# Kernel tuning notes

Measured on AMD Instinct MI355X. Metric: run time of the kernel, lower is better.

The kernel has to match this reference:

```python
import jax, jax.numpy as jnp
import numpy as np

B, L, I, O = 32, 512, 1024, 1024
TMIN, TMAX = -8.0, -2.0


def setup_inputs() -> dict:
    key = jax.random.key(0)
    k1, k2, k3, k4, k5 = jax.random.split(key, 5)
    x = jax.random.normal(k1, (B, L, I), dtype=jnp.float32)
    weight_mean = jax.random.normal(k2, (O, I), dtype=jnp.float32) * 0.02
    # matches torch init: -rand * (tmax - tmin) + tmin
    weight_logvar = -jax.random.uniform(k3, (O, I), dtype=jnp.float32) * (TMAX - TMIN) + TMIN
    bias = jax.random.normal(k4, (O,), dtype=jnp.float32) * 0.02
    # standard-normal reparameterization noise (the torch module's randn)
    noise = jax.random.normal(k5, (B, O, I), dtype=jnp.float32)
    return {"x": x, "weight_mean": weight_mean, "weight_logvar": weight_logvar,
            "bias": bias, "noise": noise}


def reference(x, weight_mean, weight_logvar, bias, noise):
    # per-sample sampled weights: W_b = mean + eps_b * sqrt(exp(logvar))
    w = weight_mean + noise * jnp.exp(0.5 * weight_logvar)  # (B, O, I)
    # bmm(x, W^T) + bias  ->  (B, L, O)
    return jnp.einsum('bli,boi->blo', x, w) + bias
```

## Files before the change

### kernel.cpp

```cpp
#include <hip/hip_runtime.h>
#include <hip/hip_bf16.h>
#include <stdint.h>

#define B_ 32
#define L_ 512
#define I_ 1024
#define O_ 1024
#define NSTEP (I_ / 32)

typedef float  f32x4  __attribute__((ext_vector_type(4)));
typedef __bf16 bf16x4 __attribute__((ext_vector_type(4)));
typedef __bf16 bf16x8 __attribute__((ext_vector_type(8)));

__device__ __forceinline__ void gload_lds16(const void* g, void* l) {
    __builtin_amdgcn_global_load_lds(
        (const __attribute__((address_space(1))) uint32_t*)(uintptr_t)g,
        (__attribute__((address_space(3))) uint32_t*)(uint32_t)(uintptr_t)l,
        16, 0, 0);
}

__global__ void gen_w_kernel(const float* __restrict__ wmean,
                             const float* __restrict__ wlv,
                             const float* __restrict__ noise,
                             __bf16* __restrict__ W)
{
    const int n4 = B_ * O_ * I_ / 4;
    const int stride = gridDim.x * blockDim.x;
    for (int i = blockIdx.x * blockDim.x + threadIdx.x; i < n4; i += stride) {
        const int mi = i & (O_ * I_ / 4 - 1);
        const f32x4 m4 = *(const f32x4*)(wmean + (size_t)mi * 4);
        const f32x4 l4 = *(const f32x4*)(wlv   + (size_t)mi * 4);
        const f32x4 e4 = *(const f32x4*)(noise + (size_t)i  * 4);
        bf16x4 w;
        w[0] = (__bf16)(m4[0] + e4[0] * __expf(0.5f * l4[0]));
        w[1] = (__bf16)(m4[1] + e4[1] * __expf(0.5f * l4[1]));
        w[2] = (__bf16)(m4[2] + e4[2] * __expf(0.5f * l4[2]));
        w[3] = (__bf16)(m4[3] + e4[3] * __expf(0.5f * l4[3]));
        *(bf16x4*)(W + (size_t)i * 4) = w;
    }
}

__global__ void cvt_x_kernel(const float* __restrict__ x, __bf16* __restrict__ xb)
{
    const int n4 = B_ * L_ * I_ / 4;
    const int stride = gridDim.x * blockDim.x;
    for (int i = blockIdx.x * blockDim.x + threadIdx.x; i < n4; i += stride) {
        const f32x4 v = *(const f32x4*)(x + (size_t)i * 4);
        bf16x4 w;
        w[0] = (__bf16)v[0]; w[1] = (__bf16)v[1];
        w[2] = (__bf16)v[2]; w[3] = (__bf16)v[3];
        *(bf16x4*)(xb + (size_t)i * 4) = w;
    }
}

__global__ __launch_bounds__(256) void gemm_2ph(const __bf16* __restrict__ xb,
                                                const __bf16* __restrict__ W,
                                                const float* __restrict__ bias,
                                                float* __restrict__ out)
{
    __shared__ __bf16 As[2][128 * 32];
    __shared__ __bf16 Bs[2][128 * 32];

    const int bid = ((int)blockIdx.x & 7) * 128 + ((int)blockIdx.x >> 3);
    const int b   = bid >> 5;
    const int mt  = (bid >> 3) & 3;
    const int nt  = bid & 7;

    const int t    = threadIdx.x;
    const int wave = t >> 6, lane = t & 63;
    const int wr   = wave >> 1, wc = wave & 1;
    const int hr   = lane & 15, kq = lane >> 4;

    const __bf16* xrow = xb + (size_t)b * L_ * I_ + (size_t)(mt * 128) * I_;
    const __bf16* wrow = W  + (size_t)b * O_ * I_ + (size_t)(nt * 128) * I_;

    const int r1 = t >> 2, q1 = t & 3;
    const size_t goff1 = (size_t)r1 * I_ + q1 * 8;
    const size_t goff2 = (size_t)(r1 + 64) * I_ + q1 * 8;

    f32x4 acc[4][4];
    #pragma unroll
    for (int m = 0; m < 4; ++m)
        #pragma unroll
        for (int n = 0; n < 4; ++n)
            acc[m][n] = (f32x4)(0.0f);

    gload_lds16(xrow + goff1, &As[0][t * 8]);
    gload_lds16(wrow + goff1, &Bs[0][t * 8]);
    gload_lds16(xrow + goff2, &As[0][t * 8 + 2048]);
    gload_lds16(wrow + goff2, &Bs[0][t * 8 + 2048]);
    __syncthreads();

    int cur = 0;
    for (int it = 0; it < NSTEP; ++it) {
        if (it + 1 < NSTEP) {
            const int k0n = (it + 1) * 32;
            const int nxt = cur ^ 1;
            gload_lds16(xrow + goff1 + k0n, &As[nxt][t * 8]);
            gload_lds16(wrow + goff1 + k0n, &Bs[nxt][t * 8]);
            gload_lds16(xrow + goff2 + k0n, &As[nxt][t * 8 + 2048]);
            gload_lds16(wrow + goff2 + k0n, &Bs[nxt][t * 8 + 2048]);
        }

        bf16x8 af[4], bfr[4];
        #pragma unroll
        for (int m = 0; m < 4; ++m)
            af[m] = *(const bf16x8*)&As[cur][(wr * 64 + m * 16 + hr) * 32 + kq * 8];
        #pragma unroll
        for (int n = 0; n < 4; ++n)
            bfr[n] = *(const bf16x8*)&Bs[cur][(wc * 64 + n * 16 + hr) * 32 + kq * 8];
        #pragma unroll
        for (int m = 0; m < 4; ++m)
            #pragma unroll
            for (int n = 0; n < 4; ++n)
                acc[m][n] = __builtin_amdgcn_mfma_f32_16x16x32_bf16(af[m], bfr[n], acc[m][n], 0, 0, 0);

        __syncthreads();
        cur ^= 1;
    }

    float* ob = out + (size_t)b * L_ * O_;
    #pragma unroll
    for (int n = 0; n < 4; ++n) {
        const int col = nt * 128 + wc * 64 + n * 16 + hr;
        const float bv = bias[col];
        #pragma unroll
        for (int m = 0; m < 4; ++m) {
            const int row0 = mt * 128 + wr * 64 + m * 16 + kq * 4;
            #pragma unroll
            for (int j = 0; j < 4; ++j)
                ob[(size_t)(row0 + j) * O_ + col] = acc[m][n][j] + bv;
        }
    }
}

#define LDSPAD 40
__global__ void bayes_gemm_fused(const float* __restrict__ x,
                                 const float* __restrict__ wmean,
                                 const float* __restrict__ wlogvar,
                                 const float* __restrict__ bias,
                                 const float* __restrict__ noise,
                                 float* __restrict__ out)
{
    __shared__ __bf16 As[128 * LDSPAD];
    __shared__ __bf16 Bs[128 * LDSPAD];
    const int bid  = blockIdx.x;
    const int b    = bid >> 5;
    const int mt   = (bid >> 3) & 3;
    const int nt   = bid & 7;
    const int t    = threadIdx.x;
    const int wave = t >> 6, lane = t & 63;
    const int wr   = wave >> 1, wc = wave & 1;
    const int hr   = lane & 15, kq = lane >> 4;
    const float* xb = x     + (size_t)b * L_ * I_;
    const float* nb = noise + (size_t)b * O_ * I_;
    f32x4 acc[4][4];
    #pragma unroll
    for (int m = 0; m < 4; ++m)
        #pragma unroll
        for (int n = 0; n < 4; ++n) acc[m][n] = (f32x4)(0.0f);
    for (int k0 = 0; k0 < I_; k0 += 32) {
        #pragma unroll
        for (int j = 0; j < 4; ++j) {
            const int s = t + j * 256, row = s >> 3, q = s & 7;
            const float4 v = *(const float4*)(xb + (size_t)(mt * 128 + row) * I_ + k0 + q * 4);
            __bf16* dst = &As[row * LDSPAD + q * 4];
            dst[0] = (__bf16)v.x; dst[1] = (__bf16)v.y; dst[2] = (__bf16)v.z; dst[3] = (__bf16)v.w;
        }
        #pragma unroll
        for (int j = 0; j < 4; ++j) {
            const int s = t + j * 256, row = s >> 3, q = s & 7;
            const size_t off = (size_t)(nt * 128 + row) * I_ + k0 + q * 4;
            const float4 m4 = *(const float4*)(wmean + off);
            const float4 l4 = *(const float4*)(wlogvar + off);
            const float4 n4 = *(const float4*)(nb + off);
            __bf16* dst = &Bs[row * LDSPAD + q * 4];
            dst[0] = (__bf16)(m4.x + n4.x * __expf(0.5f * l4.x));
            dst[1] = (__bf16)(m4.y + n4.y * __expf(0.5f * l4.y));
            dst[2] = (__bf16)(m4.z + n4.z * __expf(0.5f * l4.z));
            dst[3] = (__bf16)(m4.w + n4.w * __expf(0.5f * l4.w));
        }
        __syncthreads();
        bf16x8 af[4], bfr[4];
        #pragma unroll
        for (int m = 0; m < 4; ++m)
            af[m] = *(const bf16x8*)&As[(wr * 64 + m * 16 + hr) * LDSPAD + kq * 8];
        #pragma unroll
        for (int n = 0; n < 4; ++n)
            bfr[n] = *(const bf16x8*)&Bs[(wc * 64 + n * 16 + hr) * LDSPAD + kq * 8];
        #pragma unroll
        for (int m = 0; m < 4; ++m)
            #pragma unroll
            for (int n = 0; n < 4; ++n)
                acc[m][n] = __builtin_amdgcn_mfma_f32_16x16x32_bf16(af[m], bfr[n], acc[m][n], 0, 0, 0);
        __syncthreads();
    }
    float* ob = out + (size_t)b * L_ * O_;
    #pragma unroll
    for (int n = 0; n < 4; ++n) {
        const int col = nt * 128 + wc * 64 + n * 16 + hr;
        const float bv = bias[col];
        #pragma unroll
        for (int m = 0; m < 4; ++m) {
            const int row0 = mt * 128 + wr * 64 + m * 16 + kq * 4;
            #pragma unroll
            for (int j = 0; j < 4; ++j)
                ob[(size_t)(row0 + j) * O_ + col] = acc[m][n][j] + bv;
        }
    }
}

extern "C" void kernel_launch(void* const* d_in, const int* in_sizes, int n_in,
                              void* d_out, int out_size, void* d_ws, size_t ws_size,
                              hipStream_t stream) {
    const float* x       = (const float*)d_in[0];
    const float* wmean   = (const float*)d_in[1];
    const float* wlogvar = (const float*)d_in[2];
    const float* bias    = (const float*)d_in[3];
    const float* noise   = (const float*)d_in[4];
    float* out           = (float*)d_out;

    const size_t w_bytes  = (size_t)B_ * O_ * I_ * 2;
    const size_t xb_bytes = (size_t)B_ * L_ * I_ * 2;

    if (ws_size >= w_bytes + xb_bytes) {
        __bf16* W  = (__bf16*)d_ws;
        __bf16* xb = (__bf16*)((char*)d_ws + w_bytes);
        gen_w_kernel<<<dim3(2048), dim3(256), 0, stream>>>(wmean, wlogvar, noise, W);
        cvt_x_kernel<<<dim3(1024), dim3(256), 0, stream>>>(x, xb);
        gemm_2ph<<<dim3(1024), dim3(256), 0, stream>>>(xb, W, bias, out);
    } else {
        bayes_gemm_fused<<<dim3(1024), dim3(256), 0, stream>>>(
            x, wmean, wlogvar, bias, noise, out);
    }
}
```

Measured before the change: 124.6 us.

## Rewrite bf16 GEMM with 256x256 tiles, 4-stage LDS ring and swizzle

Replaces the double-buffered 128x128 GEMM with a 256x256 tile kernel of 512 threads. It uses a four-deep LDS ring fed by async global-to-LDS loads, explicit vmcnt waits and a single barrier per k-step. The LDS layout is XOR-swizzled to avoid bank conflicts, and s_setprio is raised around the MFMA block. The aim is higher data reuse per tile and better overlap of loads with matrix math. In exchange it uses more LDS and registers and launches only 256 blocks, which may leave some compute units underused.

Result: faster. 113.8 us (-8.7%).

```diff
diff --git a/kernel.cpp b/kernel.cpp
--- a/kernel.cpp
+++ b/kernel.cpp
@@ -6,7 +6,8 @@
 #define L_ 512
 #define I_ 1024
 #define O_ 1024
-#define NSTEP (I_ / 32)
+#define BK 32
+#define NT (I_ / BK)
 
 typedef float  f32x4  __attribute__((ext_vector_type(4)));
 typedef __bf16 bf16x4 __attribute__((ext_vector_type(4)));
@@ -53,80 +54,94 @@
     }
 }
 
-__global__ __launch_bounds__(256) void gemm_2ph(const __bf16* __restrict__ xb,
-                                                const __bf16* __restrict__ W,
-                                                const float* __restrict__ bias,
-                                                float* __restrict__ out)
-{
-    __shared__ __bf16 As[2][128 * 32];
-    __shared__ __bf16 Bs[2][128 * 32];
-
-    const int bid = ((int)blockIdx.x & 7) * 128 + ((int)blockIdx.x >> 3);
-    const int b   = bid >> 5;
-    const int mt  = (bid >> 3) & 3;
-    const int nt  = bid & 7;
-
-    const int t    = threadIdx.x;
-    const int wave = t >> 6, lane = t & 63;
-    const int wr   = wave >> 1, wc = wave & 1;
-    const int hr   = lane & 15, kq = lane >> 4;
-
-    const __bf16* xrow = xb + (size_t)b * L_ * I_ + (size_t)(mt * 128) * I_;
-    const __bf16* wrow = W  + (size_t)b * O_ * I_ + (size_t)(nt * 128) * I_;
-
-    const int r1 = t >> 2, q1 = t & 3;
-    const size_t goff1 = (size_t)r1 * I_ + q1 * 8;
-    const size_t goff2 = (size_t)(r1 + 64) * I_ + q1 * 8;
-
-    f32x4 acc[4][4];
-    #pragma unroll
-    for (int m = 0; m < 4; ++m)
+__global__ __launch_bounds__(512, 2) void gemm_ring(const __bf16* __restrict__ xb,
+                                                    const __bf16* __restrict__ W,
+                                                    const float* __restrict__ bias,
+                                                    float* __restrict__ out)
+{
+    __shared__ __bf16 Abuf[4][256 * BK];
+    __shared__ __bf16 Bbuf[4][256 * BK];
+
+    const int bid = ((int)blockIdx.x & 7) * 32 + ((int)blockIdx.x >> 3);
+    const int b   = bid >> 3;
+    const int mt  = (bid >> 2) & 1;
+    const int nt  = bid & 3;
+
+    const int tid  = threadIdx.x;
+    const int wid  = tid >> 6, lane = tid & 63;
+    const int wr   = wid >> 2;
+    const int wc   = wid & 3;
+    const int hr   = lane & 15;
+    const int kq   = lane >> 4;
+
+    const int rowS = tid >> 2;
+    const int pcS  = tid & 3;
+    const int cS   = pcS ^ ((rowS >> 1) & 3);
+    const __bf16* ga = xb + (size_t)b * L_ * I_ + (size_t)(mt * 256 + rowS) * I_ + cS * 8;
+    const __bf16* gb = W  + (size_t)b * O_ * I_ + (size_t)(nt * 256 + rowS) * I_ + cS * 8;
+    const size_t ghalf = (size_t)128 * I_;
+
+#define STAGE(kt_) {                                                        \
+        const int bsel_ = (kt_) & 3;                                        \
+        const int ko_   = (kt_) * BK;                                       \
+        gload_lds16(ga + ko_,         &Abuf[bsel_][tid * 8]);               \
+        gload_lds16(ga + ko_ + ghalf, &Abuf[bsel_][tid * 8 + 4096]);        \
+        gload_lds16(gb + ko_,         &Bbuf[bsel_][tid * 8]);               \
+        gload_lds16(gb + ko_ + ghalf, &Bbuf[bsel_][tid * 8 + 4096]);        \
+    }
+
+    const int xorv = (hr >> 1) & 3;
+    const int pch  = kq ^ xorv;
+    const int aoff = (wr * 128 + hr) * 64 + pch * 16;
+    const int boff = (wc * 64  + hr) * 64 + pch * 16;
+
+    f32x4 acc[8][4];
+    #pragma unroll
+    for (int m = 0; m < 8; ++m)
         #pragma unroll
         for (int n = 0; n < 4; ++n)
             acc[m][n] = (f32x4)(0.0f);
 
-    gload_lds16(xrow + goff1, &As[0][t * 8]);
-    gload_lds16(wrow + goff1, &Bs[0][t * 8]);
-    gload_lds16(xrow + goff2, &As[0][t * 8 + 2048]);
-    gload_lds16(wrow + goff2, &Bs[0][t * 8 + 2048]);
-    __syncthreads();
-
-    int cur = 0;
-    for (int it = 0; it < NSTEP; ++it) {
-        if (it + 1 < NSTEP) {
-            const int k0n = (it + 1) * 32;
-            const int nxt = cur ^ 1;
-            gload_lds16(xrow + goff1 + k0n, &As[nxt][t * 8]);
-            gload_lds16(wrow + goff1 + k0n, &Bs[nxt][t * 8]);
-            gload_lds16(xrow + goff2 + k0n, &As[nxt][t * 8 + 2048]);
-            gload_lds16(wrow + goff2 + k0n, &Bs[nxt][t * 8 + 2048]);
-        }
-
-        bf16x8 af[4], bfr[4];
-        #pragma unroll
-        for (int m = 0; m < 4; ++m)
-            af[m] = *(const bf16x8*)&As[cur][(wr * 64 + m * 16 + hr) * 32 + kq * 8];
+    STAGE(0); STAGE(1); STAGE(2);
+
+    for (int kt = 0; kt < NT; ++kt) {
+        if (kt <= NT - 3)      asm volatile("s_waitcnt vmcnt(8)" ::: "memory");
+        else if (kt == NT - 2) asm volatile("s_waitcnt vmcnt(4)" ::: "memory");
+        else                   asm volatile("s_waitcnt vmcnt(0)" ::: "memory");
+        __builtin_amdgcn_s_barrier();
+        asm volatile("" ::: "memory");
+
+        if (kt + 3 < NT) STAGE(kt + 3);
+
+        const char* As = (const char*)&Abuf[kt & 3][0];
+        const char* Bs = (const char*)&Bbuf[kt & 3][0];
+
+        bf16x8 af[8], bfr[4];
+        #pragma unroll
+        for (int m = 0; m < 8; ++m)
+            af[m] = *(const bf16x8*)(As + aoff + m * 1024);
         #pragma unroll
         for (int n = 0; n < 4; ++n)
-            bfr[n] = *(const bf16x8*)&Bs[cur][(wc * 64 + n * 16 + hr) * 32 + kq * 8];
-        #pragma unroll
-        for (int m = 0; m < 4; ++m)
+            bfr[n] = *(const bf16x8*)(Bs + boff + n * 1024);
+
+        __builtin_amdgcn_s_setprio(1);
+        #pragma unroll
+        for (int m = 0; m < 8; ++m)
             #pragma unroll
             for (int n = 0; n < 4; ++n)
                 acc[m][n] = __builtin_amdgcn_mfma_f32_16x16x32_bf16(af[m], bfr[n], acc[m][n], 0, 0, 0);
-
-        __syncthreads();
-        cur ^= 1;
-    }
+        __builtin_amdgcn_s_setprio(0);
+    }
+#undef STAGE
 
     float* ob = out + (size_t)b * L_ * O_;
     #pragma unroll
     for (int n = 0; n < 4; ++n) {
-        const int col = nt * 128 + wc * 64 + n * 16 + hr;
+        const int col = nt * 256 + wc * 64 + n * 16 + hr;
         const float bv = bias[col];
         #pragma unroll
-        for (int m = 0; m < 4; ++m) {
-            const int row0 = mt * 128 + wr * 64 + m * 16 + kq * 4;
+        for (int m = 0; m < 8; ++m) {
+            const int row0 = mt * 256 + wr * 128 + m * 16 + kq * 4;
             #pragma unroll
             for (int j = 0; j < 4; ++j)
                 ob[(size_t)(row0 + j) * O_ + col] = acc[m][n][j] + bv;
@@ -225,10 +240,10 @@
 
     if (ws_size >= w_bytes + xb_bytes) {
         __bf16* W  = (__bf16*)d_ws;
-        __bf16* xb = (__bf16*)((char*)d_ws + w_bytes);
+        __bf16* xbuf = (__bf16*)((char*)d_ws + w_bytes);
         gen_w_kernel<<<dim3(2048), dim3(256), 0, stream>>>(wmean, wlogvar, noise, W);
-        cvt_x_kernel<<<dim3(1024), dim3(256), 0, stream>>>(x, xb);
-        gemm_2ph<<<dim3(1024), dim3(256), 0, stream>>>(xb, W, bias, out);
+        cvt_x_kernel<<<dim3(1024), dim3(256), 0, stream>>>(x, xbuf);
+        gemm_ring<<<dim3(256), dim3(512), 0, stream>>>(xbuf, W, bias, out);
     } else {
         bayes_gemm_fused<<<dim3(1024), dim3(256), 0, stream>>>(
             x, wmean, wlogvar, bias, noise, out);
```

## Fuse weight sampling and x conversion into GEMM with precomputed bf16 mean/sigma

Applied to the files above, without the earlier changes.

Replaces the three-kernel pipeline (materialize sampled bf16 W for all batches, convert x to bf16, then GEMM) with a small kernel that precomputes bf16 mean and sigma once, plus a fused GEMM. The fused GEMM reads fp32 x and noise directly, forms the sampled weights in registers, and writes bf16 tiles to double-buffered padded LDS. It uses 512-thread blocks, an LDS-staged coalesced epilogue, and raised wave priority around the MFMAs. This removes the large intermediate W and xb writes and re-reads. The cost is extra per-tile conversion work inside the GEMM and register-staged loads in place of direct global-to-LDS loads. Rounding mean and sigma to bf16 before combining them also slightly changes precision.

Result: slower. 136.4 us (+9.5%).

```diff
diff --git a/kernel.cpp b/kernel.cpp
--- a/kernel.cpp
+++ b/kernel.cpp
@@ -6,130 +6,158 @@
 #define L_ 512
 #define I_ 1024
 #define O_ 1024
-#define NSTEP (I_ / 32)
-
-typedef float  f32x4  __attribute__((ext_vector_type(4)));
+#define NST 32
+
+typedef float  f32x4 __attribute__((ext_vector_type(4)));
+typedef float  f32x2 __attribute__((ext_vector_type(2)));
 typedef __bf16 bf16x4 __attribute__((ext_vector_type(4)));
 typedef __bf16 bf16x8 __attribute__((ext_vector_type(8)));
 
-__device__ __forceinline__ void gload_lds16(const void* g, void* l) {
-    __builtin_amdgcn_global_load_lds(
-        (const __attribute__((address_space(1))) uint32_t*)(uintptr_t)g,
-        (__attribute__((address_space(3))) uint32_t*)(uint32_t)(uintptr_t)l,
-        16, 0, 0);
-}
-
-__global__ void gen_w_kernel(const float* __restrict__ wmean,
-                             const float* __restrict__ wlv,
-                             const float* __restrict__ noise,
-                             __bf16* __restrict__ W)
+#define CFENCE() asm volatile("" ::: "memory")
+#define BARRIER() do { CFENCE(); __builtin_amdgcn_s_barrier(); CFENCE(); } while (0)
+#define LGKM0()  asm volatile("s_waitcnt lgkmcnt(0)" ::: "memory")
+
+__global__ void gen_ms_kernel(const float* __restrict__ wmean, const float* __restrict__ wlv,
+                              __bf16* __restrict__ mz, __bf16* __restrict__ sgm)
 {
-    const int n4 = B_ * O_ * I_ / 4;
-    const int stride = gridDim.x * blockDim.x;
-    for (int i = blockIdx.x * blockDim.x + threadIdx.x; i < n4; i += stride) {
-        const int mi = i & (O_ * I_ / 4 - 1);
-        const f32x4 m4 = *(const f32x4*)(wmean + (size_t)mi * 4);
-        const f32x4 l4 = *(const f32x4*)(wlv   + (size_t)mi * 4);
-        const f32x4 e4 = *(const f32x4*)(noise + (size_t)i  * 4);
-        bf16x4 w;
-        w[0] = (__bf16)(m4[0] + e4[0] * __expf(0.5f * l4[0]));
-        w[1] = (__bf16)(m4[1] + e4[1] * __expf(0.5f * l4[1]));
-        w[2] = (__bf16)(m4[2] + e4[2] * __expf(0.5f * l4[2]));
-        w[3] = (__bf16)(m4[3] + e4[3] * __expf(0.5f * l4[3]));
-        *(bf16x4*)(W + (size_t)i * 4) = w;
-    }
-}
-
-__global__ void cvt_x_kernel(const float* __restrict__ x, __bf16* __restrict__ xb)
+    const int i = blockIdx.x * blockDim.x + threadIdx.x;
+    const f32x4 m = *(const f32x4*)(wmean + (size_t)i * 4);
+    const f32x4 l = *(const f32x4*)(wlv   + (size_t)i * 4);
+    bf16x4 mb, sb;
+    #pragma unroll
+    for (int e = 0; e < 4; ++e) {
+        mb[e] = (__bf16)m[e];
+        sb[e] = (__bf16)__expf(0.5f * l[e]);
+    }
+    *(bf16x4*)(mz  + (size_t)i * 4) = mb;
+    *(bf16x4*)(sgm + (size_t)i * 4) = sb;
+}
+
+__global__ __launch_bounds__(512, 4) void fused_gemm(const float* __restrict__ x,
+                                                     const float* __restrict__ noise,
+                                                     const __bf16* __restrict__ mz,
+                                                     const __bf16* __restrict__ sgm,
+                                                     const float* __restrict__ bias,
+                                                     float* __restrict__ out)
 {
-    const int n4 = B_ * L_ * I_ / 4;
-    const int stride = gridDim.x * blockDim.x;
-    for (int i = blockIdx.x * blockDim.x + threadIdx.x; i < n4; i += stride) {
-        const f32x4 v = *(const f32x4*)(x + (size_t)i * 4);
-        bf16x4 w;
-        w[0] = (__bf16)v[0]; w[1] = (__bf16)v[1];
-        w[2] = (__bf16)v[2]; w[3] = (__bf16)v[3];
-        *(bf16x4*)(xb + (size_t)i * 4) = w;
-    }
-}
-
-__global__ __launch_bounds__(256) void gemm_2ph(const __bf16* __restrict__ xb,
-                                                const __bf16* __restrict__ W,
-                                                const float* __restrict__ bias,
-                                                float* __restrict__ out)
-{
-    __shared__ __bf16 As[2][128 * 32];
-    __shared__ __bf16 Bs[2][128 * 32];
+    __shared__ __align__(16) char smem[40960];
 
     const int bid = ((int)blockIdx.x & 7) * 128 + ((int)blockIdx.x >> 3);
     const int b   = bid >> 5;
     const int mt  = (bid >> 3) & 3;
     const int nt  = bid & 7;
 
-    const int t    = threadIdx.x;
-    const int wave = t >> 6, lane = t & 63;
-    const int wr   = wave >> 1, wc = wave & 1;
-    const int hr   = lane & 15, kq = lane >> 4;
-
-    const __bf16* xrow = xb + (size_t)b * L_ * I_ + (size_t)(mt * 128) * I_;
-    const __bf16* wrow = W  + (size_t)b * O_ * I_ + (size_t)(nt * 128) * I_;
-
-    const int r1 = t >> 2, q1 = t & 3;
-    const size_t goff1 = (size_t)r1 * I_ + q1 * 8;
-    const size_t goff2 = (size_t)(r1 + 64) * I_ + q1 * 8;
-
-    f32x4 acc[4][4];
-    #pragma unroll
-    for (int m = 0; m < 4; ++m)
+    const int tid  = threadIdx.x;
+    const int wid  = tid >> 6, lane = tid & 63;
+    const int wr   = wid >> 1;
+    const int wc   = wid & 1;
+    const int hr   = lane & 15;
+    const int kq   = lane >> 4;
+
+    const int rS = tid >> 2, kc = tid & 3;
+    const float*  xg = x     + ((size_t)b * L_ + mt * 128 + rS) * I_ + kc * 8;
+    const float*  ng = noise + ((size_t)b * O_ + nt * 128 + rS) * I_ + kc * 8;
+    const __bf16* mg = mz    + (size_t)(nt * 128 + rS) * I_ + kc * 8;
+    const __bf16* gg = sgm   + (size_t)(nt * 128 + rS) * I_ + kc * 8;
+    const int wbyte = rS * 80 + kc * 16;
+
+    f32x4 sa0, sa1, sn0, sn1; bf16x8 sm, ss;
+
+#define ISSUE(k0_) do {                                       \
+        sa0 = *(const f32x4*)(xg + (k0_));                    \
+        sa1 = *(const f32x4*)(xg + (k0_) + 4);                \
+        sn0 = *(const f32x4*)(ng + (k0_));                    \
+        sn1 = *(const f32x4*)(ng + (k0_) + 4);                \
+        sm  = *(const bf16x8*)(mg + (k0_));                   \
+        ss  = *(const bf16x8*)(gg + (k0_));                   \
+    } while (0)
+
+#define TW(d_) do {                                                        \
+        bf16x8 aw_, ww_;                                                   \
+        _Pragma("unroll")                                                  \
+        for (int e = 0; e < 4; ++e) {                                      \
+            aw_[e]   = (__bf16)sa0[e];                                     \
+            aw_[e+4] = (__bf16)sa1[e];                                     \
+            ww_[e]   = (__bf16)((float)sm[e]   + sn0[e] * (float)ss[e]);   \
+            ww_[e+4] = (__bf16)((float)sm[e+4] + sn1[e] * (float)ss[e+4]); \
+        }                                                                  \
+        *(bf16x8*)(smem + (d_) * 20480 + wbyte)         = aw_;             \
+        *(bf16x8*)(smem + (d_) * 20480 + 10240 + wbyte) = ww_;             \
+    } while (0)
+
+    const int aoff0 = (wr * 32 + 0 * 16 + hr) * 80 + kq * 16;
+    const int aoff1 = (wr * 32 + 1 * 16 + hr) * 80 + kq * 16;
+    int boff[4];
+    #pragma unroll
+    for (int nf = 0; nf < 4; ++nf)
+        boff[nf] = 10240 + (wc * 64 + nf * 16 + hr) * 80 + kq * 16;
+
+    f32x4 acc[2][4];
+    #pragma unroll
+    for (int m = 0; m < 2; ++m)
         #pragma unroll
         for (int n = 0; n < 4; ++n)
             acc[m][n] = (f32x4)(0.0f);
 
-    gload_lds16(xrow + goff1, &As[0][t * 8]);
-    gload_lds16(wrow + goff1, &Bs[0][t * 8]);
-    gload_lds16(xrow + goff2, &As[0][t * 8 + 2048]);
-    gload_lds16(wrow + goff2, &Bs[0][t * 8 + 2048]);
-    __syncthreads();
-
-    int cur = 0;
-    for (int it = 0; it < NSTEP; ++it) {
-        if (it + 1 < NSTEP) {
-            const int k0n = (it + 1) * 32;
-            const int nxt = cur ^ 1;
-            gload_lds16(xrow + goff1 + k0n, &As[nxt][t * 8]);
-            gload_lds16(wrow + goff1 + k0n, &Bs[nxt][t * 8]);
-            gload_lds16(xrow + goff2 + k0n, &As[nxt][t * 8 + 2048]);
-            gload_lds16(wrow + goff2 + k0n, &Bs[nxt][t * 8 + 2048]);
-        }
-
-        bf16x8 af[4], bfr[4];
-        #pragma unroll
-        for (int m = 0; m < 4; ++m)
-            af[m] = *(const bf16x8*)&As[cur][(wr * 64 + m * 16 + hr) * 32 + kq * 8];
-        #pragma unroll
-        for (int n = 0; n < 4; ++n)
-            bfr[n] = *(const bf16x8*)&Bs[cur][(wc * 64 + n * 16 + hr) * 32 + kq * 8];
-        #pragma unroll
-        for (int m = 0; m < 4; ++m)
+    ISSUE(0);
+    TW(0);
+    ISSUE(32);
+    LGKM0();
+    BARRIER();
+
+    for (int t = 0; t < NST; ++t) {
+        const int d = t & 1;
+        const char* base = smem + d * 20480;
+
+        bf16x8 af0 = *(const bf16x8*)(base + aoff0);
+        bf16x8 af1 = *(const bf16x8*)(base + aoff1);
+        bf16x8 bf[4];
+        #pragma unroll
+        for (int nf = 0; nf < 4; ++nf)
+            bf[nf] = *(const bf16x8*)(base + boff[nf]);
+
+        __builtin_amdgcn_s_setprio(1);
+        #pragma unroll
+        for (int nf = 0; nf < 4; ++nf) {
+            acc[0][nf] = __builtin_amdgcn_mfma_f32_16x16x32_bf16(af0, bf[nf], acc[0][nf], 0, 0, 0);
+            acc[1][nf] = __builtin_amdgcn_mfma_f32_16x16x32_bf16(af1, bf[nf], acc[1][nf], 0, 0, 0);
+        }
+        __builtin_amdgcn_s_setprio(0);
+
+        if (t + 1 < NST) TW(d ^ 1);
+        if (t + 2 < NST) ISSUE((t + 2) * 32);
+        LGKM0();
+        BARRIER();
+    }
+#undef ISSUE
+#undef TW
+
+    {
+        float* eb = (float*)smem;
+        const f32x2 bias2 = *(const f32x2*)(bias + nt * 128 + lane * 2);
+        float* ob = out + ((size_t)b * L_ + mt * 128) * O_ + nt * 128;
+        #pragma unroll
+        for (int r = 0; r < 2; ++r) {
+            BARRIER();
+            if ((wr >> 1) == r) {
+                #pragma unroll
+                for (int mf = 0; mf < 2; ++mf)
+                    #pragma unroll
+                    for (int nf = 0; nf < 4; ++nf) {
+                        const int col = wc * 64 + nf * 16 + hr;
+                        #pragma unroll
+                        for (int j = 0; j < 4; ++j)
+                            eb[((wr & 1) * 32 + mf * 16 + kq * 4 + j) * 130 + col] = acc[mf][nf][j];
+                    }
+            }
+            BARRIER();
             #pragma unroll
-            for (int n = 0; n < 4; ++n)
-                acc[m][n] = __builtin_amdgcn_mfma_f32_16x16x32_bf16(af[m], bfr[n], acc[m][n], 0, 0, 0);
-
-        __syncthreads();
-        cur ^= 1;
-    }
-
-    float* ob = out + (size_t)b * L_ * O_;
-    #pragma unroll
-    for (int n = 0; n < 4; ++n) {
-        const int col = nt * 128 + wc * 64 + n * 16 + hr;
-        const float bv = bias[col];
-        #pragma unroll
-        for (int m = 0; m < 4; ++m) {
-            const int row0 = mt * 128 + wr * 64 + m * 16 + kq * 4;
-            #pragma unroll
-            for (int j = 0; j < 4; ++j)
-                ob[(size_t)(row0 + j) * O_ + col] = acc[m][n][j] + bv;
+            for (int rr = 0; rr < 8; ++rr) {
+                const int row = wid * 8 + rr;
+                f32x2 v = *(const f32x2*)&eb[row * 130 + lane * 2];
+                v[0] += bias2[0]; v[1] += bias2[1];
+                *(f32x2*)&ob[(size_t)(r * 64 + row) * O_ + lane * 2] = v;
+            }
         }
     }
 }
@@ -220,15 +248,13 @@
     const float* noise   = (const float*)d_in[4];
     float* out           = (float*)d_out;
 
-    const size_t w_bytes  = (size_t)B_ * O_ * I_ * 2;
-    const size_t xb_bytes = (size_t)B_ * L_ * I_ * 2;
-
-    if (ws_size >= w_bytes + xb_bytes) {
-        __bf16* W  = (__bf16*)d_ws;
-        __bf16* xb = (__bf16*)((char*)d_ws + w_bytes);
-        gen_w_kernel<<<dim3(2048), dim3(256), 0, stream>>>(wmean, wlogvar, noise, W);
-        cvt_x_kernel<<<dim3(1024), dim3(256), 0, stream>>>(x, xb);
-        gemm_2ph<<<dim3(1024), dim3(256), 0, stream>>>(xb, W, bias, out);
+    const size_t ms_bytes = (size_t)O_ * I_ * 2 * 2;
+
+    if (ws_size >= ms_bytes) {
+        __bf16* mzb = (__bf16*)d_ws;
+        __bf16* sgb = mzb + (size_t)O_ * I_;
+        gen_ms_kernel<<<dim3(O_ * I_ / 4 / 256), dim3(256), 0, stream>>>(wmean, wlogvar, mzb, sgb);
+        fused_gemm<<<dim3(1024), dim3(512), 0, stream>>>(x, noise, mzb, sgb, bias, out);
     } else {
         bayes_gemm_fused<<<dim3(1024), dim3(256), 0, stream>>>(
             x, wmean, wlogvar, bias, noise, out);
```

## Triple-buffer GEMM LDS pipeline and stage epilogue through LDS for coalesced stores

Applied to the files above, without the earlier changes.

Replaces the double-buffered GEMM with a three-stage LDS ring that prefetches two K-tiles ahead. It uses explicit vmcnt waits and a single barrier per iteration instead of two syncthreads, and raises wave priority around the MFMA block. The epilogue now goes through LDS so each wave writes contiguous float2 rows with the bias added, replacing strided scalar stores. This uses more LDS per block, which may lower occupancy, and the hand-written waitcnt values must match the number of loads in flight.

Result: no change. 123.9 us (-0.5%).

```diff
diff --git a/kernel.cpp b/kernel.cpp
--- a/kernel.cpp
+++ b/kernel.cpp
@@ -6,11 +6,16 @@
 #define L_ 512
 #define I_ 1024
 #define O_ 1024
-#define NSTEP (I_ / 32)
-
-typedef float  f32x4  __attribute__((ext_vector_type(4)));
+#define NT 32
+
+typedef float  f32x4 __attribute__((ext_vector_type(4)));
+typedef float  f32x2 __attribute__((ext_vector_type(2)));
 typedef __bf16 bf16x4 __attribute__((ext_vector_type(4)));
 typedef __bf16 bf16x8 __attribute__((ext_vector_type(8)));
+
+#define CFENCE() asm volatile("" ::: "memory")
+#define BARRIER() do { CFENCE(); __builtin_amdgcn_s_barrier(); CFENCE(); } while (0)
+#define LGKM0()  asm volatile("s_waitcnt lgkmcnt(0)" ::: "memory")
 
 __device__ __forceinline__ void gload_lds16(const void* g, void* l) {
     __builtin_amdgcn_global_load_lds(
@@ -53,30 +58,45 @@
     }
 }
 
-__global__ __launch_bounds__(256) void gemm_2ph(const __bf16* __restrict__ xb,
-                                                const __bf16* __restrict__ W,
-                                                const float* __restrict__ bias,
-                                                float* __restrict__ out)
-{
-    __shared__ __bf16 As[2][128 * 32];
-    __shared__ __bf16 Bs[2][128 * 32];
+__global__ __launch_bounds__(256) void gemm_r3(const __bf16* __restrict__ xb,
+                                               const __bf16* __restrict__ W,
+                                               const float* __restrict__ bias,
+                                               float* __restrict__ out)
+{
+    __shared__ __align__(16) char smem[49152];
 
     const int bid = ((int)blockIdx.x & 7) * 128 + ((int)blockIdx.x >> 3);
     const int b   = bid >> 5;
     const int mt  = (bid >> 3) & 3;
     const int nt  = bid & 7;
 
-    const int t    = threadIdx.x;
-    const int wave = t >> 6, lane = t & 63;
-    const int wr   = wave >> 1, wc = wave & 1;
-    const int hr   = lane & 15, kq = lane >> 4;
-
-    const __bf16* xrow = xb + (size_t)b * L_ * I_ + (size_t)(mt * 128) * I_;
-    const __bf16* wrow = W  + (size_t)b * O_ * I_ + (size_t)(nt * 128) * I_;
-
-    const int r1 = t >> 2, q1 = t & 3;
-    const size_t goff1 = (size_t)r1 * I_ + q1 * 8;
-    const size_t goff2 = (size_t)(r1 + 64) * I_ + q1 * 8;
+    const int tid  = threadIdx.x;
+    const int wave = tid >> 6, lane = tid & 63;
+    const int wr   = wave >> 1;
+    const int wc   = wave & 1;
+    const int hr   = lane & 15;
+    const int kq   = lane >> 4;
+
+    const int rS = tid >> 2, kc = tid & 3;
+    const size_t H64 = (size_t)64 * I_;
+    const __bf16* xrow = xb + ((size_t)b * L_ + mt * 128 + rS) * I_ + kc * 8;
+    const __bf16* wrow = W  + ((size_t)b * O_ + nt * 128 + rS) * I_ + kc * 8;
+
+#define STG(kt_) do {                                                     \
+        char* sl_ = smem + ((kt_) % 3) * 16384;                           \
+        const int ko_ = (kt_) * 32;                                       \
+        gload_lds16(xrow + ko_,        sl_ + tid * 16);                   \
+        gload_lds16(xrow + ko_ + H64,  sl_ + 4096 + tid * 16);            \
+        gload_lds16(wrow + ko_,        sl_ + 8192 + tid * 16);            \
+        gload_lds16(wrow + ko_ + H64,  sl_ + 12288 + tid * 16);           \
+    } while (0)
+
+    int aoff[4], boff[4];
+    #pragma unroll
+    for (int f = 0; f < 4; ++f) {
+        aoff[f] = (wr * 64 + f * 16 + hr) * 64 + kq * 16;
+        boff[f] = 8192 + (wc * 64 + f * 16 + hr) * 64 + kq * 16;
+    }
 
     f32x4 acc[4][4];
     #pragma unroll
@@ -85,51 +105,61 @@
         for (int n = 0; n < 4; ++n)
             acc[m][n] = (f32x4)(0.0f);
 
-    gload_lds16(xrow + goff1, &As[0][t * 8]);
-    gload_lds16(wrow + goff1, &Bs[0][t * 8]);
-    gload_lds16(xrow + goff2, &As[0][t * 8 + 2048]);
-    gload_lds16(wrow + goff2, &Bs[0][t * 8 + 2048]);
-    __syncthreads();
-
-    int cur = 0;
-    for (int it = 0; it < NSTEP; ++it) {
-        if (it + 1 < NSTEP) {
-            const int k0n = (it + 1) * 32;
-            const int nxt = cur ^ 1;
-            gload_lds16(xrow + goff1 + k0n, &As[nxt][t * 8]);
-            gload_lds16(wrow + goff1 + k0n, &Bs[nxt][t * 8]);
-            gload_lds16(xrow + goff2 + k0n, &As[nxt][t * 8 + 2048]);
-            gload_lds16(wrow + goff2 + k0n, &Bs[nxt][t * 8 + 2048]);
-        }
-
+    STG(0);
+    STG(1);
+
+    for (int t = 0; t < NT; ++t) {
+        if (t + 1 < NT) { CFENCE(); asm volatile("s_waitcnt vmcnt(4)" ::: "memory"); }
+        else           { CFENCE(); asm volatile("s_waitcnt vmcnt(0)" ::: "memory"); }
+        BARRIER();
+
+        if (t + 2 < NT) STG(t + 2);
+
+        const char* base = smem + (t % 3) * 16384;
         bf16x8 af[4], bfr[4];
         #pragma unroll
-        for (int m = 0; m < 4; ++m)
-            af[m] = *(const bf16x8*)&As[cur][(wr * 64 + m * 16 + hr) * 32 + kq * 8];
-        #pragma unroll
-        for (int n = 0; n < 4; ++n)
-            bfr[n] = *(const bf16x8*)&Bs[cur][(wc * 64 + n * 16 + hr) * 32 + kq * 8];
+        for (int f = 0; f < 4; ++f) {
+            af[f]  = *(const bf16x8*)(base + aoff[f]);
+            bfr[f] = *(const bf16x8*)(base + boff[f]);
+        }
+
+        __builtin_amdgcn_s_setprio(1);
         #pragma unroll
         for (int m = 0; m < 4; ++m)
             #pragma unroll
             for (int n = 0; n < 4; ++n)
                 acc[m][n] = __builtin_amdgcn_mfma_f32_16x16x32_bf16(af[m], bfr[n], acc[m][n], 0, 0, 0);
-
-        __syncthreads();
-        cur ^= 1;
-    }
-
-    float* ob = out + (size_t)b * L_ * O_;
-    #pragma unroll
-    for (int n = 0; n < 4; ++n) {
-        const int col = nt * 128 + wc * 64 + n * 16 + hr;
-        const float bv = bias[col];
-        #pragma unroll
-        for (int m = 0; m < 4; ++m) {
-            const int row0 = mt * 128 + wr * 64 + m * 16 + kq * 4;
-            #pragma unroll
-            for (int j = 0; j < 4; ++j)
-                ob[(size_t)(row0 + j) * O_ + col] = acc[m][n][j] + bv;
+        __builtin_amdgcn_s_setprio(0);
+    }
+#undef STG
+
+    {
+        float* eb = (float*)smem;
+        const f32x2 bias2 = *(const f32x2*)(bias + nt * 128 + lane * 2);
+        float* ob = out + ((size_t)b * L_ + mt * 128) * O_ + nt * 128;
+        #pragma unroll
+        for (int r = 0; r < 2; ++r) {
+            BARRIER();
+            if (wr == r) {
+                #pragma unroll
+                for (int m = 0; m < 4; ++m)
+                    #pragma unroll
+                    for (int n = 0; n < 4; ++n) {
+                        const int col = wc * 64 + n * 16 + hr;
+                        #pragma unroll
+                        for (int j = 0; j < 4; ++j)
+                            eb[(m * 16 + kq * 4 + j) * 130 + col] = acc[m][n][j];
+                    }
+            }
+            LGKM0();
+            BARRIER();
+            #pragma unroll
+            for (int rr = 0; rr < 16; ++rr) {
+                const int row = wave * 16 + rr;
+                f32x2 v = *(const f32x2*)&eb[row * 130 + lane * 2];
+                v[0] += bias2[0]; v[1] += bias2[1];
+                *(f32x2*)&ob[(size_t)(r * 64 + row) * O_ + lane * 2] = v;
+            }
         }
     }
 }
@@ -224,11 +254,11 @@
     const size_t xb_bytes = (size_t)B_ * L_ * I_ * 2;
 
     if (ws_size >= w_bytes + xb_bytes) {
-        __bf16* W  = (__bf16*)d_ws;
-        __bf16* xb = (__bf16*)((char*)d_ws + w_bytes);
+        __bf16* W    = (__bf16*)d_ws;
+        __bf16* xbuf = (__bf16*)((char*)d_ws + w_bytes);
         gen_w_kernel<<<dim3(2048), dim3(256), 0, stream>>>(wmean, wlogvar, noise, W);
-        cvt_x_kernel<<<dim3(1024), dim3(256), 0, stream>>>(x, xb);
-        gemm_2ph<<<dim3(1024), dim3(256), 0, stream>>>(xb, W, bias, out);
+        cvt_x_kernel<<<dim3(1024), dim3(256), 0, stream>>>(x, xbuf);
+        gemm_r3<<<dim3(1024), dim3(256), 0, stream>>>(xbuf, W, bias, out);
     } else {
         bayes_gemm_fused<<<dim3(1024), dim3(256), 0, stream>>>(
             x, wmean, wlogvar, bias, noise, out);
```
